# Optimization experiments

Hardware: AMD Instinct MI355X
Metric: run time of the kernel (lower is better)

The kernel has to match this reference:

```python
import jax, jax.numpy as jnp
import numpy as np

B, S, E, H = 2, 2048, 1024, 16
HD = E // H


def setup_inputs() -> dict:
    key = jax.random.key(0)
    ks = jax.random.split(key, 5)
    scale = 1.0 / np.sqrt(E)
    return {
        "x": jax.random.normal(ks[0], (B, S, E), dtype=jnp.float32),
        "Wq": jax.random.normal(ks[1], (H, HD, E), dtype=jnp.float32) * scale,
        "Wk": jax.random.normal(ks[2], (H, HD, E), dtype=jnp.float32) * scale,
        "Wv": jax.random.normal(ks[3], (H, HD, E), dtype=jnp.float32) * scale,
        "Wo": jax.random.normal(ks[4], (E, E), dtype=jnp.float32) * scale,
    }


def reference(x, Wq, Wk, Wv, Wo):
    # Batched per-head projections: torch Linear y = x @ W.T, W: [head_dim, E]
    q = jnp.einsum("bse,hde->bshd", x, Wq)  # [B,S,H,HD]
    k = jnp.einsum("bse,hde->bshd", x, Wk)
    v = jnp.einsum("bse,hde->bshd", x, Wv)
    # Scaled dot-product attention; original scales by sqrt(head_dim)
    scores = jnp.einsum("bqhd,bkhd->bhqk", q, k) / jnp.sqrt(jnp.float32(HD))
    attn = jax.nn.softmax(scores, axis=-1)  # [B,H,S,S]
    out_h = jnp.einsum("bhqk,bkhd->bqhd", attn, v)  # [B,S,H,HD]
    out_cat = out_h.reshape(x.shape[0], x.shape[1], -1)  # concat heads -> [B,S,E]
    return out_cat @ Wo.T
```

## Files before the change

### kernel.cpp

```cpp
#include <hip/hip_runtime.h>
#include <hip/hip_bf16.h>

typedef unsigned short u16;
typedef unsigned int u32;
typedef __attribute__((ext_vector_type(4))) float f32x4;
typedef __attribute__((ext_vector_type(16))) float f32x16;
typedef __attribute__((ext_vector_type(8))) short short8;
typedef __attribute__((ext_vector_type(8))) unsigned short u16x8;
typedef __attribute__((ext_vector_type(4))) unsigned short u16x4;
typedef __attribute__((ext_vector_type(4))) unsigned int u32x4;

#define BATCH 2
#define SEQ   2048
#define EMB   1024
#define NH    16
#define HD    64

__device__ inline u16 f2bf(float f) {
    unsigned u = __builtin_bit_cast(unsigned, f);
    unsigned r = u + 0x7FFFu + ((u >> 16) & 1u);
    return (u16)(r >> 16);
}

__device__ inline float fexp2(float x) {
    float r;
    asm("v_exp_f32 %0, %1" : "=v"(r) : "v"(x));
    return r;
}

__device__ inline void gload16(const void* g, void* l) {
    __builtin_amdgcn_global_load_lds(
        (const __attribute__((address_space(1))) unsigned int*)g,
        (__attribute__((address_space(3))) unsigned int*)l, 16, 0, 0);
}

__device__ inline short8 mk8(u32 a, u32 b, u32 c, u32 d) {
    u32x4 t; t[0] = a; t[1] = b; t[2] = c; t[3] = d;
    return __builtin_bit_cast(short8, t);
}

#define PACK_ST(st, w0,w1,w2,w3,w4,w5,w6,w7)                                   \
  {                                                                            \
    asm("v_cvt_pk_bf16_f32 %0, %1, %2" : "=v"(w0) : "v"(st[0]),  "v"(st[1]));  \
    asm("v_cvt_pk_bf16_f32 %0, %1, %2" : "=v"(w1) : "v"(st[2]),  "v"(st[3]));  \
    asm("v_cvt_pk_bf16_f32 %0, %1, %2" : "=v"(w2) : "v"(st[4]),  "v"(st[5]));  \
    asm("v_cvt_pk_bf16_f32 %0, %1, %2" : "=v"(w3) : "v"(st[6]),  "v"(st[7]));  \
    asm("v_permlane32_swap_b32 %0, %1" : "+v"(w0), "+v"(w2));                  \
    asm("v_permlane32_swap_b32 %0, %1" : "+v"(w1), "+v"(w3));                  \
    asm("v_cvt_pk_bf16_f32 %0, %1, %2" : "=v"(w4) : "v"(st[8]),  "v"(st[9]));  \
    asm("v_cvt_pk_bf16_f32 %0, %1, %2" : "=v"(w5) : "v"(st[10]), "v"(st[11])); \
    asm("v_cvt_pk_bf16_f32 %0, %1, %2" : "=v"(w6) : "v"(st[12]), "v"(st[13])); \
    asm("v_cvt_pk_bf16_f32 %0, %1, %2" : "=v"(w7) : "v"(st[14]), "v"(st[15])); \
    asm("v_permlane32_swap_b32 %0, %1" : "+v"(w4), "+v"(w6));                  \
    asm("v_permlane32_swap_b32 %0, %1" : "+v"(w5), "+v"(w7));                  \
  }

__global__ __launch_bounds__(256) void convert_all(
    const float* __restrict__ x,
    const float* __restrict__ Wq, const float* __restrict__ Wk, const float* __restrict__ Wv,
    u16* __restrict__ Xb, u16* __restrict__ Wqkv)
{
    const long gidx = (long)blockIdx.x * 2048 + (long)threadIdx.x * 8;
    const float* src;
    u16* dst;
    if (gidx < 4194304L) {
        src = x + gidx; dst = Xb + gidx;
    } else {
        const long r = gidx - 4194304L;
        const int w = (int)(r >> 20);
        const long off = r & 1048575L;
        src = (w == 0 ? Wq : w == 1 ? Wk : Wv) + off;
        dst = Wqkv + r;
    }
    f32x4 a = *(const f32x4*)src;
    f32x4 b = *(const f32x4*)(src + 4);
    u16x8 o;
    #pragma unroll
    for (int j = 0; j < 4; ++j) { o[j] = f2bf(a[j]); o[4 + j] = f2bf(b[j]); }
    *(u16x8*)dst = o;
}

__global__ __launch_bounds__(256) void convert_wo(
    const float* __restrict__ Wo, u16* __restrict__ Wob)
{
    const long gidx = (long)blockIdx.x * 2048 + (long)threadIdx.x * 8;
    f32x4 a = *(const f32x4*)(Wo + gidx);
    f32x4 b = *(const f32x4*)(Wo + gidx + 4);
    u16x8 o;
    #pragma unroll
    for (int j = 0; j < 4; ++j) { o[j] = f2bf(a[j]); o[4 + j] = f2bf(b[j]); }
    *(u16x8*)(Wob + gidx) = o;
}

__global__ __launch_bounds__(512, 2) void gemm256(
    const u16* __restrict__ A, const u16* __restrict__ Bb,
    u16* __restrict__ Qo, u16* __restrict__ Ko, u16* __restrict__ VTo)
{
    __shared__ u16 As[2][256 * 64];
    __shared__ u16 Bs[2][256 * 64];

    const int tid = threadIdx.x;
    const int lane = tid & 63;
    const int wid = tid >> 6;
    const int lr = lane & 15;
    const int lg = lane >> 4;
    const int wr = wid >> 2;
    const int wc = wid & 3;

    const int lin = blockIdx.y * 16 + blockIdx.x;
    const int swz = (lin & 7) * 24 + (lin >> 3);
    const int m0 = (swz & 15) * 256;
    const int n0 = (swz >> 4) * 256;

    const int grow = lane >> 3;
    const int schunk = ((lane & 7) ^ grow) << 4;

    auto issueTile = [&](int kt, int buf) {
        const int k0b = kt * 128;
        #pragma unroll
        for (int i = 0; i < 4; ++i) {
            const int row = i * 64 + wid * 8 + grow;
            gload16((const char*)A + (size_t)(m0 + row) * 2048 + k0b + schunk,
                    (char*)As[buf] + i * 8192 + wid * 1024);
            gload16((const char*)Bb + (size_t)(n0 + row) * 2048 + k0b + schunk,
                    (char*)Bs[buf] + i * 8192 + wid * 1024);
        }
    };

    issueTile(0, 0);
    issueTile(1, 1);

    f32x4 acc[8][4] = {};
    const int rsw = (lr & 7);

    for (int t = 0; t < 16; ++t) {
        if (t < 15) { asm volatile("s_waitcnt vmcnt(8)" ::: "memory"); }
        else        { asm volatile("s_waitcnt vmcnt(0)" ::: "memory"); }
        __builtin_amdgcn_sched_barrier(0);
        __builtin_amdgcn_s_barrier();
        __builtin_amdgcn_sched_barrier(0);

        const u16* Ac = As[t & 1];
        const u16* Bc = Bs[t & 1];

        short8 a[4][2], b0[2][2], b1[2][2];

        #pragma unroll
        for (int fi = 0; fi < 4; ++fi)
            #pragma unroll
            for (int ks = 0; ks < 2; ++ks)
                a[fi][ks] = *(const short8*)((const char*)Ac + (wr * 128 + fi * 16 + lr) * 128
                                             + (((ks * 4 + lg) ^ rsw) << 4));
        #pragma unroll
        for (int fj = 0; fj < 2; ++fj)
            #pragma unroll
            for (int ks = 0; ks < 2; ++ks)
                b0[fj][ks] = *(const short8*)((const char*)Bc + (wc * 64 + fj * 16 + lr) * 128
                                              + (((ks * 4 + lg) ^ rsw) << 4));
        __builtin_amdgcn_s_setprio(1);
        #pragma unroll
        for (int fi = 0; fi < 4; ++fi)
            #pragma unroll
            for (int fj = 0; fj < 2; ++fj)
                #pragma unroll
                for (int ks = 0; ks < 2; ++ks)
                    acc[fi][fj] = __builtin_amdgcn_mfma_f32_16x16x32_bf16(a[fi][ks], b0[fj][ks], acc[fi][fj], 0, 0, 0);
        __builtin_amdgcn_s_setprio(0);

        #pragma unroll
        for (int fj = 0; fj < 2; ++fj)
            #pragma unroll
            for (int ks = 0; ks < 2; ++ks)
                b1[fj][ks] = *(const short8*)((const char*)Bc + (wc * 64 + (fj + 2) * 16 + lr) * 128
                                              + (((ks * 4 + lg) ^ rsw) << 4));
        __builtin_amdgcn_s_setprio(1);
        #pragma unroll
        for (int fi = 0; fi < 4; ++fi)
            #pragma unroll
            for (int fj = 0; fj < 2; ++fj)
                #pragma unroll
                for (int ks = 0; ks < 2; ++ks)
                    acc[fi][fj + 2] = __builtin_amdgcn_mfma_f32_16x16x32_bf16(a[fi][ks], b1[fj][ks], acc[fi][fj + 2], 0, 0, 0);
        __builtin_amdgcn_s_setprio(0);

        #pragma unroll
        for (int fi = 0; fi < 4; ++fi)
            #pragma unroll
            for (int ks = 0; ks < 2; ++ks)
                a[fi][ks] = *(const short8*)((const char*)Ac + (wr * 128 + (fi + 4) * 16 + lr) * 128
                                             + (((ks * 4 + lg) ^ rsw) << 4));
        __builtin_amdgcn_s_setprio(1);
        #pragma unroll
        for (int fi = 0; fi < 4; ++fi)
            #pragma unroll
            for (int fj = 0; fj < 2; ++fj)
                #pragma unroll
                for (int ks = 0; ks < 2; ++ks)
                    acc[fi + 4][fj + 2] = __builtin_amdgcn_mfma_f32_16x16x32_bf16(a[fi][ks], b1[fj][ks], acc[fi + 4][fj + 2], 0, 0, 0);
        __builtin_amdgcn_s_setprio(0);

        __builtin_amdgcn_s_setprio(1);
        #pragma unroll
        for (int fi = 0; fi < 4; ++fi)
            #pragma unroll
            for (int fj = 0; fj < 2; ++fj)
                #pragma unroll
                for (int ks = 0; ks < 2; ++ks)
                    acc[fi + 4][fj] = __builtin_amdgcn_mfma_f32_16x16x32_bf16(a[fi][ks], b0[fj][ks], acc[fi + 4][fj], 0, 0, 0);
        __builtin_amdgcn_s_setprio(0);

        __builtin_amdgcn_sched_barrier(0);
        __builtin_amdgcn_s_barrier();
        __builtin_amdgcn_sched_barrier(0);
        if (t + 2 < 16) issueTile(t + 2, t & 1);
    }

    const int w = n0 >> 10;
    const float qs = (w == 0) ? 0.125f * 1.44269504f : 1.0f;
    const int mb = m0 + wr * 128;
    const int nb = n0 + wc * 64;
    #pragma unroll
    for (int fi = 0; fi < 8; ++fi) {
        #pragma unroll
        for (int fj = 0; fj < 4; ++fj) {
            const int m = mb + fi * 16 + lg * 4;
            const int nn = (nb + fj * 16 + lr) & 1023;
            const int h = nn >> 6, d = nn & 63;
            const int bb = m >> 11, s = m & 2047;
            const size_t bh = (size_t)(bb * NH + h);
            if (w == 2) {
                u16x4 v;
                #pragma unroll
                for (int i = 0; i < 4; ++i) v[i] = f2bf(acc[fi][fj][i]);
                *(u16x4*)&VTo[(bh * HD + d) * SEQ + s] = v;
            } else {
                u16* P = (w == 0) ? Qo : Ko;
                #pragma unroll
                for (int i = 0; i < 4; ++i)
                    P[(bh * SEQ + s + i) * HD + d] = f2bf(acc[fi][fj][i] * qs);
            }
        }
    }
}

__global__ __launch_bounds__(256) void gemm_out(
    const u16* __restrict__ A, const u16* __restrict__ Bb, float* __restrict__ Fo)
{
    __shared__ u16 As[2][128 * 64];
    __shared__ u16 Bs[2][128 * 64];

    const int tid = threadIdx.x;

    const int lin = blockIdx.y * 32 + blockIdx.x;
    const int swz = (lin & 7) * 32 + (lin >> 3);
    const int m0 = (swz & 31) * 128;
    const int n0 = (swz >> 5) * 128;

    const int lane = tid & 63;
    const int lr = lane & 15;
    const int lg = lane >> 4;
    const int wid = tid >> 6;
    const int wm = wid >> 1, wn = wid & 1;

    const int grow = lane >> 3;
    const int gcolb = ((lane & 7) ^ grow) << 4;
    const int rswz = (lr & 7);

    f32x4 acc[4][4] = {};

    auto issue = [&](int kt, int buf) {
        const int k0b = kt * 128;
        #pragma unroll
        for (int t = 0; t < 4; ++t) {
            const int row = (wid * 4 + t) * 8 + grow;
            gload16((const char*)A + (size_t)(m0 + row) * 2048 + k0b + gcolb,
                    (char*)As[buf] + (wid * 4 + t) * 1024);
            gload16((const char*)Bb + (size_t)(n0 + row) * 2048 + k0b + gcolb,
                    (char*)Bs[buf] + (wid * 4 + t) * 1024);
        }
    };

    issue(0, 0);
    issue(1, 1);

    for (int kt = 0; kt < 16; ++kt) {
        if (kt < 15) { asm volatile("s_waitcnt vmcnt(8)" ::: "memory"); }
        else         { asm volatile("s_waitcnt vmcnt(0)" ::: "memory"); }
        __builtin_amdgcn_sched_barrier(0);
        __builtin_amdgcn_s_barrier();
        __builtin_amdgcn_sched_barrier(0);

        const u16* Ac = As[kt & 1];
        const u16* Bc = Bs[kt & 1];
        #pragma unroll
        for (int kk = 0; kk < 2; ++kk) {
            short8 a[4], b[4];
            #pragma unroll
            for (int i = 0; i < 4; ++i)
                a[i] = *(const short8*)((const char*)Ac + (wm * 64 + i * 16 + lr) * 128
                                        + (((kk * 4 + lg) ^ rswz) << 4));
            #pragma unroll
            for (int i = 0; i < 4; ++i)
                b[i] = *(const short8*)((const char*)Bc + (wn * 64 + i * 16 + lr) * 128
                                        + (((kk * 4 + lg) ^ rswz) << 4));
            #pragma unroll
            for (int mi = 0; mi < 4; ++mi)
                #pragma unroll
                for (int ni = 0; ni < 4; ++ni)
                    acc[mi][ni] = __builtin_amdgcn_mfma_f32_16x16x32_bf16(a[mi], b[ni], acc[mi][ni], 0, 0, 0);
        }

        __builtin_amdgcn_sched_barrier(0);
        __builtin_amdgcn_s_barrier();
        __builtin_amdgcn_sched_barrier(0);
        if (kt + 2 < 16) issue(kt + 2, kt & 1);
    }

    const int mb = m0 + wm * 64;
    const int nb = n0 + wn * 64;
    #pragma unroll
    for (int mi = 0; mi < 4; ++mi)
        #pragma unroll
        for (int ni = 0; ni < 4; ++ni) {
            const int m = mb + mi * 16 + lg * 4;
            const int n = nb + ni * 16 + lr;
            #pragma unroll
            for (int i = 0; i < 4; ++i)
                Fo[(size_t)(m + i) * EMB + n] = acc[mi][ni][i];
        }
}

__global__ __launch_bounds__(256) void attn_fwd(
    const u16* __restrict__ Q, const u16* __restrict__ K,
    const u16* __restrict__ VT, u16* __restrict__ Cat)
{
    __shared__ u16 Ks[4][64 * 64];
    __shared__ u16 Vs[4][64 * 64];

    const int tid = threadIdx.x;
    const int lane = tid & 63;
    const int wid = tid >> 6;
    const int lq = lane & 31;
    const int hi = lane >> 5;

    const int lin = blockIdx.y * 16 + blockIdx.x;
    const int swz = (lin & 7) * 64 + (lin >> 3);
    const int qt = swz & 15;
    const int bh = swz >> 4;
    const int b = bh >> 4, h = bh & 15;

    const u16* Qg = Q + ((size_t)bh * SEQ + qt * 128 + wid * 32 + lq) * HD;
    short8 qf[4];
    #pragma unroll
    for (int ks = 0; ks < 4; ++ks)
        qf[ks] = *(const short8*)((const char*)Qg + ks * 32 + hi * 16);

    float lsum = 0.f;
    f32x16 ot0 = {}, ot1 = {};

    const u16* Kg = K + (size_t)bh * SEQ * HD;
    const u16* Vg = VT + (size_t)bh * HD * SEQ;

    const int srow = lane >> 3;
    const int schunk = ((lane & 7) ^ srow) << 4;

    auto issueKV = [&](int nt) {
        const int kv0 = nt * 64;
        #pragma unroll
        for (int i = 0; i < 2; ++i) {
            const int krow = i * 32 + wid * 8 + srow;
            gload16((const char*)Kg + (size_t)(kv0 + krow) * 128 + schunk,
                    (char*)Ks[nt & 3] + i * 4096 + wid * 1024);
            gload16((const char*)Vg + (size_t)krow * (SEQ * 2) + kv0 * 2 + schunk,
                    (char*)Vs[nt & 3] + i * 4096 + wid * 1024);
        }
    };

    const int rsw = (lq & 7);

    auto tile = [&](const u16* Kbuf, const u16* Vbuf) {
        f32x16 st0 = {}, st1 = {};
        #pragma unroll
        for (int ks = 0; ks < 4; ++ks) {
            const int co = ((ks * 2 + hi) ^ rsw) << 4;
            const short8 kf0 = *(const short8*)((const char*)Kbuf + lq * 128 + co);
            const short8 kf1 = *(const short8*)((const char*)Kbuf + (32 + lq) * 128 + co);
            st0 = __builtin_amdgcn_mfma_f32_32x32x16_bf16(kf0, qf[ks], st0, 0, 0, 0);
            st1 = __builtin_amdgcn_mfma_f32_32x32x16_bf16(kf1, qf[ks], st1, 0, 0, 0);
        }

        #pragma unroll
        for (int i = 0; i < 16; ++i) {
            st0[i] = fexp2(st0[i]);
            st1[i] = fexp2(st1[i]);
        }
        float s0 = 0.f, s1 = 0.f, s2 = 0.f, s3 = 0.f;
        #pragma unroll
        for (int i = 0; i < 16; i += 4) {
            s0 += st0[i]     + st1[i];
            s1 += st0[i + 1] + st1[i + 1];
            s2 += st0[i + 2] + st1[i + 2];
            s3 += st0[i + 3] + st1[i + 3];
        }
        lsum += (s0 + s1) + (s2 + s3);

        u32 a0, a1, a2, a3, a4, a5, a6, a7;
        u32 c0, c1, c2, c3, c4, c5, c6, c7;
        PACK_ST(st0, a0, a1, a2, a3, a4, a5, a6, a7);
        PACK_ST(st1, c0, c1, c2, c3, c4, c5, c6, c7);
        const short8 pf0 = mk8(a0, a1, a2, a3);
        const short8 pf1 = mk8(a4, a5, a6, a7);
        const short8 pf2 = mk8(c0, c1, c2, c3);
        const short8 pf3 = mk8(c4, c5, c6, c7);

        #pragma unroll
        for (int ks = 0; ks < 4; ++ks) {
            const short8 pf = (ks == 0) ? pf0 : (ks == 1) ? pf1 : (ks == 2) ? pf2 : pf3;
            const int co = ((ks * 2 + hi) ^ rsw) << 4;
            const short8 vf0 = *(const short8*)((const char*)Vbuf + lq * 128 + co);
            const short8 vf1 = *(const short8*)((const char*)Vbuf + (32 + lq) * 128 + co);
            ot0 = __builtin_amdgcn_mfma_f32_32x32x16_bf16(vf0, pf, ot0, 0, 0, 0);
            ot1 = __builtin_amdgcn_mfma_f32_32x32x16_bf16(vf1, pf, ot1, 0, 0, 0);
        }
    };

    issueKV(0); issueKV(1); issueKV(2); issueKV(3);

    for (int p = 0; p < 16; ++p) {
        if (p < 15) { asm volatile("s_waitcnt vmcnt(8)" ::: "memory"); }
        else        { asm volatile("s_waitcnt vmcnt(0)" ::: "memory"); }
        __builtin_amdgcn_sched_barrier(0);
        __builtin_amdgcn_s_barrier();
        __builtin_amdgcn_sched_barrier(0);

        const int c0 = (p & 1) << 1;
        tile(Ks[c0], Vs[c0]);
        tile(Ks[c0 + 1], Vs[c0 + 1]);

        __builtin_amdgcn_sched_barrier(0);
        __builtin_amdgcn_s_barrier();
        __builtin_amdgcn_sched_barrier(0);
        const int t4 = 2 * p + 4;
        if (t4 < 32)     issueKV(t4);
        if (t4 + 1 < 32) issueKV(t4 + 1);
    }

    const float l = lsum + __shfl_xor(lsum, 32);
    const float invl = 1.f / l;
    const int qrow = qt * 128 + wid * 32 + lq;
    u16* ob = Cat + ((size_t)b * SEQ + qrow) * EMB + h * HD;
    #pragma unroll
    for (int g = 0; g < 4; ++g) {
        u16x4 o0, o1;
        #pragma unroll
        for (int i = 0; i < 4; ++i) {
            o0[i] = f2bf(ot0[g * 4 + i] * invl);
            o1[i] = f2bf(ot1[g * 4 + i] * invl);
        }
        *(u16x4*)&ob[g * 8 + hi * 4] = o0;
        *(u16x4*)&ob[32 + g * 8 + hi * 4] = o1;
    }
}

extern "C" void kernel_launch(void* const* d_in, const int* in_sizes, int n_in,
                              void* d_out, int out_size, void* d_ws, size_t ws_size,
                              hipStream_t stream) {
    const float* x  = (const float*)d_in[0];
    const float* Wq = (const float*)d_in[1];
    const float* Wk = (const float*)d_in[2];
    const float* Wv = (const float*)d_in[3];
    const float* Wo = (const float*)d_in[4];
    float* out = (float*)d_out;

    u16* Xb   = (u16*)d_out;
    u16* Wqkv = (u16*)d_out + (size_t)4 * 1048576;

    char* ws = (char*)d_ws;
    u16* Qb  = (u16*)(ws);
    u16* Kb  = (u16*)(ws + (size_t)8  * 1048576);
    u16* VTb = (u16*)(ws + (size_t)16 * 1048576);
    u16* Cat = (u16*)(ws + (size_t)24 * 1048576);
    u16* Wob = Qb;

    convert_all<<<3584, 256, 0, stream>>>(x, Wq, Wk, Wv, Xb, Wqkv);

    dim3 g1(4096 / 256, 3072 / 256);
    gemm256<<<g1, 512, 0, stream>>>(Xb, Wqkv, Qb, Kb, VTb);

    dim3 g2(SEQ / 128, BATCH * NH);
    attn_fwd<<<g2, 256, 0, stream>>>(Qb, Kb, VTb, Cat);

    convert_wo<<<512, 256, 0, stream>>>(Wo, Wob);
    dim3 g3(4096 / 128, 1024 / 128);
    gemm_out<<<g3, 256, 0, stream>>>(Cat, Wob, out);
}
```

Before: 123.9 us.

## Load K/V fragments directly from global memory, dropping the LDS pipeline

Removes the shared-memory staging of K and V tiles, including the 4-deep async load ring and its block barriers. Each wave now reads its MFMA operand fragments straight from global memory (relying on L1/L2 for reuse across the 4 waves) inside a simple loop unrolled by 2. This cuts LDS traffic and barrier synchronization but gives up the explicit prefetch overlap, so global load latency may be exposed and the redundant per-wave reads raise cache pressure.

Result: slower. 193.7 us (+56.4%).

```diff
diff --git a/kernel.cpp b/kernel.cpp
--- a/kernel.cpp
+++ b/kernel.cpp
@@ -334,9 +334,6 @@
     const u16* __restrict__ Q, const u16* __restrict__ K,
     const u16* __restrict__ VT, u16* __restrict__ Cat)
 {
-    __shared__ u16 Ks[4][64 * 64];
-    __shared__ u16 Vs[4][64 * 64];
-
     const int tid = threadIdx.x;
     const int lane = tid & 63;
     const int wid = tid >> 6;
@@ -361,32 +358,36 @@
     const u16* Kg = K + (size_t)bh * SEQ * HD;
     const u16* Vg = VT + (size_t)bh * HD * SEQ;
 
-    const int srow = lane >> 3;
-    const int schunk = ((lane & 7) ^ srow) << 4;
-
-    auto issueKV = [&](int nt) {
+    const u16* kr0 = Kg + (size_t)lq * HD;
+    const u16* kr1 = Kg + (size_t)(32 + lq) * HD;
+    const u16* vr0 = Vg + (size_t)lq * SEQ;
+    const u16* vr1 = Vg + (size_t)(32 + lq) * SEQ;
+
+    #pragma unroll 2
+    for (int nt = 0; nt < 32; ++nt) {
         const int kv0 = nt * 64;
-        #pragma unroll
-        for (int i = 0; i < 2; ++i) {
-            const int krow = i * 32 + wid * 8 + srow;
-            gload16((const char*)Kg + (size_t)(kv0 + krow) * 128 + schunk,
-                    (char*)Ks[nt & 3] + i * 4096 + wid * 1024);
-            gload16((const char*)Vg + (size_t)krow * (SEQ * 2) + kv0 * 2 + schunk,
-                    (char*)Vs[nt & 3] + i * 4096 + wid * 1024);
-        }
-    };
-
-    const int rsw = (lq & 7);
-
-    auto tile = [&](const u16* Kbuf, const u16* Vbuf) {
+
+        short8 kfa[4], kfb[4];
+        #pragma unroll
+        for (int ks = 0; ks < 4; ++ks) {
+            const int ch = (ks * 2 + hi) * 8;
+            kfa[ks] = *(const short8*)(kr0 + (size_t)kv0 * HD + ch);
+            kfb[ks] = *(const short8*)(kr1 + (size_t)kv0 * HD + ch);
+        }
+
         f32x16 st0 = {}, st1 = {};
         #pragma unroll
         for (int ks = 0; ks < 4; ++ks) {
-            const int co = ((ks * 2 + hi) ^ rsw) << 4;
-            const short8 kf0 = *(const short8*)((const char*)Kbuf + lq * 128 + co);
-            const short8 kf1 = *(const short8*)((const char*)Kbuf + (32 + lq) * 128 + co);
-            st0 = __builtin_amdgcn_mfma_f32_32x32x16_bf16(kf0, qf[ks], st0, 0, 0, 0);
-            st1 = __builtin_amdgcn_mfma_f32_32x32x16_bf16(kf1, qf[ks], st1, 0, 0, 0);
+            st0 = __builtin_amdgcn_mfma_f32_32x32x16_bf16(kfa[ks], qf[ks], st0, 0, 0, 0);
+            st1 = __builtin_amdgcn_mfma_f32_32x32x16_bf16(kfb[ks], qf[ks], st1, 0, 0, 0);
+        }
+
+        short8 vfa[4], vfb[4];
+        #pragma unroll
+        for (int ks = 0; ks < 4; ++ks) {
+            const int ch = kv0 + (ks * 2 + hi) * 8;
+            vfa[ks] = *(const short8*)(vr0 + ch);
+            vfb[ks] = *(const short8*)(vr1 + ch);
         }
 
         #pragma unroll
@@ -416,33 +417,9 @@
         #pragma unroll
         for (int ks = 0; ks < 4; ++ks) {
             const short8 pf = (ks == 0) ? pf0 : (ks == 1) ? pf1 : (ks == 2) ? pf2 : pf3;
-            const int co = ((ks * 2 + hi) ^ rsw) << 4;
-            const short8 vf0 = *(const short8*)((const char*)Vbuf + lq * 128 + co);
-            const short8 vf1 = *(const short8*)((const char*)Vbuf + (32 + lq) * 128 + co);
-            ot0 = __builtin_amdgcn_mfma_f32_32x32x16_bf16(vf0, pf, ot0, 0, 0, 0);
-            ot1 = __builtin_amdgcn_mfma_f32_32x32x16_bf16(vf1, pf, ot1, 0, 0, 0);
-        }
-    };
-
-    issueKV(0); issueKV(1); issueKV(2); issueKV(3);
-
-    for (int p = 0; p < 16; ++p) {
-        if (p < 15) { asm volatile("s_waitcnt vmcnt(8)" ::: "memory"); }
-        else        { asm volatile("s_waitcnt vmcnt(0)" ::: "memory"); }
-        __builtin_amdgcn_sched_barrier(0);
-        __builtin_amdgcn_s_barrier();
-        __builtin_amdgcn_sched_barrier(0);
-
-        const int c0 = (p & 1) << 1;
-        tile(Ks[c0], Vs[c0]);
-        tile(Ks[c0 + 1], Vs[c0 + 1]);
-
-        __builtin_amdgcn_sched_barrier(0);
-        __builtin_amdgcn_s_barrier();
-        __builtin_amdgcn_sched_barrier(0);
-        const int t4 = 2 * p + 4;
-        if (t4 < 32)     issueKV(t4);
-        if (t4 + 1 < 32) issueKV(t4 + 1);
+            ot0 = __builtin_amdgcn_mfma_f32_32x32x16_bf16(vfa[ks], pf, ot0, 0, 0, 0);
+            ot1 = __builtin_amdgcn_mfma_f32_32x32x16_bf16(vfb[ks], pf, ot1, 0, 0, 0);
+        }
     }
 
     const float l = lsum + __shfl_xor(lsum, 32);
```
